# Optimization experiments

Hardware: AMD Instinct MI355X
Metric: run time of the kernel (lower is better)

The kernel has to match this reference:

```python
import jax, jax.numpy as jnp
import numpy as np

D_MODEL = 1024
NUM_LAYERS = 4
VOCAB = 32000
NUM_HEADS = 8
HEAD_DIM = D_MODEL // NUM_HEADS
FFN_DIM = 2048
BATCH = 4
SEQ = 1024
LN_EPS = 1e-5
ROPE_THETA = 10000.0


def setup_inputs() -> dict:
    key = jax.random.key(0)
    ks = iter(jax.random.split(key, 32))
    std = 0.02
    L, D, H, Dh, F, V = NUM_LAYERS, D_MODEL, NUM_HEADS, HEAD_DIM, FFN_DIM, VOCAB
    inp = {
        "tokens": jax.random.randint(next(ks), (BATCH, SEQ), 0, V, dtype=jnp.int32),
        "emb": jax.random.normal(next(ks), (V, D), jnp.float32),
        # per-layer stacked params; Linear weights stored pre-transposed (in, out)
        "Wqkv": jax.random.normal(next(ks), (L, D, 3 * D), jnp.float32) * std,
        "bqkv": jnp.zeros((L, 3 * D), jnp.float32),
        "Wo": jax.random.normal(next(ks), (L, D, D), jnp.float32) * std,
        "bo": jnp.zeros((L, D), jnp.float32),
        "ln1_g": jnp.ones((L, D), jnp.float32),
        "ln1_b": jnp.zeros((L, D), jnp.float32),
        "ln2_g": jnp.ones((L, D), jnp.float32),
        "ln2_b": jnp.zeros((L, D), jnp.float32),
        "W1": jax.random.normal(next(ks), (L, D, F), jnp.float32) * std,
        "b1": jnp.zeros((L, F), jnp.float32),
        "W2": jax.random.normal(next(ks), (L, F, D), jnp.float32) * std,
        "b2": jnp.zeros((L, D), jnp.float32),
        "lnf_g": jnp.ones((D,), jnp.float32),
        "lnf_b": jnp.zeros((D,), jnp.float32),
        "Wout": jax.random.normal(next(ks), (D, V), jnp.float32) * std,
        "bout": jnp.zeros((V,), jnp.float32),
    }
    return inp


def _layernorm(x, g, b):
    mu = jnp.mean(x, -1, keepdims=True)
    var = jnp.mean(jnp.square(x - mu), -1, keepdims=True)
    return (x - mu) * jax.lax.rsqrt(var + LN_EPS) * g + b


def _rope_cos_sin(seq, dh, dtype):
    inv_freq = 1.0 / (ROPE_THETA ** (jnp.arange(0, dh, 2, dtype=jnp.float32) / dh))
    t = jnp.arange(seq, dtype=jnp.float32)
    freqs = jnp.outer(t, inv_freq)                      # [S, Dh/2]
    emb = jnp.concatenate([freqs, freqs], axis=-1)      # [S, Dh]
    return jnp.cos(emb).astype(dtype), jnp.sin(emb).astype(dtype)


def _rotate_half(x):
    x1, x2 = jnp.split(x, 2, axis=-1)
    return jnp.concatenate([-x2, x1], axis=-1)


def _apply_rope(x, cos, sin):
    # x: [B,S,H,Dh]; cos/sin: [S,Dh] -> broadcast over batch and heads
    return x * cos[None, :, None, :] + _rotate_half(x) * sin[None, :, None, :]


def reference(tokens, emb, Wqkv, bqkv, Wo, bo, ln1_g, ln1_b, ln2_g, ln2_b,
              W1, b1, W2, b2, lnf_g, lnf_b, Wout, bout):
    B, S = tokens.shape
    H, Dh = NUM_HEADS, HEAD_DIM
    x = emb[tokens]                                      # [B,S,D]
    cos, sin = _rope_cos_sin(S, Dh, x.dtype)
    causal = jnp.tril(jnp.ones((S, S), dtype=bool))      # True = keep
    scale = 1.0 / jnp.sqrt(jnp.asarray(Dh, x.dtype))

    def layer(xc, p):
        (wqkv, bq, wo, bo_, g1, b1_, g2, b2_, w1, bb1, w2, bb2) = p
        y = _layernorm(xc, g1, b1_)
        qkv = (y @ wqkv + bq).reshape(B, S, 3, H, Dh)
        q, k, v = qkv[:, :, 0], qkv[:, :, 1], qkv[:, :, 2]
        q = _apply_rope(q, cos, sin)
        k = _apply_rope(k, cos, sin)
        scores = jnp.einsum("bshd,bthd->bhst", q, k) * scale
        scores = jnp.where(causal[None, None], scores, -jnp.inf)
        attn = jax.nn.softmax(scores, axis=-1)
        ctx = jnp.einsum("bhst,bthd->bshd", attn, v).reshape(B, S, H * Dh)
        xc = xc + ctx @ wo + bo_
        z = _layernorm(xc, g2, b2_)
        ff = jax.nn.gelu(z @ w1 + bb1, approximate=False) @ w2 + bb2
        return xc + ff, None

    params = (Wqkv, bqkv, Wo, bo, ln1_g, ln1_b, ln2_g, ln2_b, W1, b1, W2, b2)
    x, _ = jax.lax.scan(layer, x, params)
    x = _layernorm(x, lnf_g, lnf_b)
    return x @ Wout + bout                                # [B,S,V]
```

## Files before the change

kernel.cpp:

```cpp
#include <hip/hip_runtime.h>
#include <hip/hip_bf16.h>
#include <math.h>


#define D_MODEL 1024
#define SEQ     1024
#define BATCH   4
#define NHEAD   8
#define HDIM    128
#define FFN     2048
#define NLAYER  4
#define VOCAB   32000
#define MROWS   (BATCH*SEQ)

typedef unsigned short ushort_t;
typedef __attribute__((ext_vector_type(8))) short s16x8;
typedef __attribute__((ext_vector_type(4))) float f32x4;

__device__ __forceinline__ ushort_t f2bf(float f) {
    union { float f; unsigned int u; } c; c.f = f;
    unsigned int u = c.u;
    unsigned int r = (u + 0x7FFFu + ((u >> 16) & 1u)) >> 16;
    return (ushort_t)r;
}
__device__ __forceinline__ float bf2f(ushort_t u) {
    union { unsigned int u; float f; } c; c.u = ((unsigned int)u) << 16; return c.f;
}

__device__ __forceinline__ void gload16(const void* g, void* l) {
    __builtin_amdgcn_global_load_lds(
        (const __attribute__((address_space(1))) unsigned int*)g,
        (__attribute__((address_space(3))) unsigned int*)l, 16, 0, 0);
}

__device__ __forceinline__ float gelu_exact(float x) {
    return 0.5f * x * (1.0f + erff(x * 0.70710678118654752f));
}

__global__ __launch_bounds__(256) void embed_kernel(
    const int* __restrict__ tokens, const float* __restrict__ emb,
    float* __restrict__ X)
{
    int row = blockIdx.x;
    int t = tokens[row];
    const float4* src = (const float4*)(emb + (size_t)t * D_MODEL);
    float4* dst = (float4*)(X + (size_t)row * D_MODEL);
    dst[threadIdx.x] = src[threadIdx.x];
}

__global__ __launch_bounds__(256) void ln_kernel(
    const float* __restrict__ X, const float* __restrict__ g,
    const float* __restrict__ b, ushort_t* __restrict__ Y)
{
    __shared__ float red[8];
    int row = blockIdx.x;
    const float4* x4 = (const float4*)(X + (size_t)row * D_MODEL);
    float4 v = x4[threadIdx.x];
    float s  = v.x + v.y + v.z + v.w;
    float ss = v.x*v.x + v.y*v.y + v.z*v.z + v.w*v.w;
    #pragma unroll
    for (int o = 32; o > 0; o >>= 1) { s += __shfl_down(s, o); ss += __shfl_down(ss, o); }
    int wid = threadIdx.x >> 6;
    if ((threadIdx.x & 63) == 0) { red[wid] = s; red[wid + 4] = ss; }
    __syncthreads();
    float tot  = red[0] + red[1] + red[2] + red[3];
    float tot2 = red[4] + red[5] + red[6] + red[7];
    float mu  = tot * (1.0f / D_MODEL);
    float var = tot2 * (1.0f / D_MODEL) - mu * mu;
    float r = rsqrtf(var + 1e-5f);
    const float4* g4 = (const float4*)g;
    const float4* b4 = (const float4*)b;
    float4 gv = g4[threadIdx.x], bv = b4[threadIdx.x];
    ushort4 o;
    o.x = f2bf((v.x - mu) * r * gv.x + bv.x);
    o.y = f2bf((v.y - mu) * r * gv.y + bv.y);
    o.z = f2bf((v.z - mu) * r * gv.z + bv.z);
    o.w = f2bf((v.w - mu) * r * gv.w + bv.w);
    ((ushort4*)(Y + (size_t)row * D_MODEL))[threadIdx.x] = o;
}

__global__ __launch_bounds__(256) void wconv(
    const float* __restrict__ W, ushort_t* __restrict__ Wt, int K, int N)
{
    __shared__ float t[32][33];
    const float* Wl = W + (size_t)blockIdx.z * K * N;
    ushort_t* Wtl = Wt + (size_t)blockIdx.z * K * N;
    int k0 = blockIdx.y * 32, n0 = blockIdx.x * 32;
    int tid = threadIdx.x;
    int r = tid >> 3, c4 = (tid & 7) * 4;
    float4 v = *(const float4*)(Wl + (size_t)(k0 + r) * N + n0 + c4);
    t[r][c4+0] = v.x; t[r][c4+1] = v.y; t[r][c4+2] = v.z; t[r][c4+3] = v.w;
    __syncthreads();
    ushort4 o;
    o.x = f2bf(t[c4+0][r]); o.y = f2bf(t[c4+1][r]);
    o.z = f2bf(t[c4+2][r]); o.w = f2bf(t[c4+3][r]);
    *(ushort4*)(Wtl + (size_t)(n0 + r) * K + k0 + c4) = o;
}

template<int ACT, int BETA, int OBF>
__global__ __launch_bounds__(256) void gemm_mid(
    const ushort_t* __restrict__ A, const ushort_t* __restrict__ Bt,
    const float* __restrict__ bias, float* __restrict__ Cf,
    ushort_t* __restrict__ Cb, int M, int N, int K)
{
    __shared__ __align__(16) ushort_t As[2][128 * 64];
    __shared__ __align__(16) ushort_t Bs[2][128 * 64];
    int tid = threadIdx.x, lane = tid & 63, w = tid >> 6;
    int wm = w >> 1, wn = w & 1;
    int m0 = blockIdx.x * 128, n0 = blockIdx.y * 128;
    int lr = lane & 15, kg = lane >> 4;
    const int NKT = K / 64;

    f32x4 acc[4][4] = {};

    int srow = w * 8 + (lane >> 3);
    int scol = (((lane & 7) ^ ((lane >> 3) & 7))) * 8;

    int rsw = lr & 7;
    int ch0 = (kg    ) ^ rsw;
    int ch1 = (kg + 4) ^ rsw;

#define STAGE_A(db, ht, ktile) do { \
    const ushort_t* s_ = A + (size_t)(m0 + (ht) * 64 + srow) * K + (size_t)(ktile) * 64 + scol; \
    gload16(s_,                  &As[db][((ht) * 64 + w * 8) * 64]); \
    gload16(s_ + (size_t)32 * K, &As[db][((ht) * 64 + 32 + w * 8) * 64]); \
} while (0)
#define STAGE_B(db, ht, ktile) do { \
    const ushort_t* s_ = Bt + (size_t)(n0 + (ht) * 64 + srow) * K + (size_t)(ktile) * 64 + scol; \
    gload16(s_,                  &Bs[db][((ht) * 64 + w * 8) * 64]); \
    gload16(s_ + (size_t)32 * K, &Bs[db][((ht) * 64 + 32 + w * 8) * 64]); \
} while (0)
#define SBAR() do { __builtin_amdgcn_sched_barrier(0); \
    __builtin_amdgcn_s_barrier(); __builtin_amdgcn_sched_barrier(0); } while (0)

    STAGE_A(0, 0, 0); STAGE_A(0, 1, 0); STAGE_B(0, 0, 0); STAGE_B(0, 1, 0);
    STAGE_A(1, 0, 1);
    asm volatile("s_waitcnt vmcnt(2)" ::: "memory");
    SBAR();

    for (int kt = 0; kt < NKT; ++kt) {
        int d = kt & 1, dn = d ^ 1;
        const ushort_t* pa0 = &As[d][(wm * 64 + lr) * 64 + ch0 * 8];
        const ushort_t* pa1 = &As[d][(wm * 64 + lr) * 64 + ch1 * 8];
        const ushort_t* pb0 = &Bs[d][(wn * 64 + lr) * 64 + ch0 * 8];
        const ushort_t* pb1 = &Bs[d][(wn * 64 + lr) * 64 + ch1 * 8];
        s16x8 a[4][2], b[4][2];

        #pragma unroll
        for (int mi = 0; mi < 4; ++mi) {
            a[mi][0] = *(const s16x8*)(pa0 + mi * 1024);
            a[mi][1] = *(const s16x8*)(pa1 + mi * 1024);
        }
        #pragma unroll
        for (int ni = 0; ni < 4; ++ni) {
            b[ni][0] = *(const s16x8*)(pb0 + ni * 1024);
            b[ni][1] = *(const s16x8*)(pb1 + ni * 1024);
        }
        if (kt + 1 < NKT) STAGE_A(dn, 1, kt + 1);
        __builtin_amdgcn_sched_barrier(0);

        __builtin_amdgcn_s_setprio(1);
        #pragma unroll
        for (int mi = 0; mi < 2; ++mi)
            #pragma unroll
            for (int ni = 0; ni < 2; ++ni)
                #pragma unroll
                for (int kk = 0; kk < 2; ++kk)
                    acc[mi][ni] = __builtin_amdgcn_mfma_f32_16x16x32_bf16(
                        a[mi][kk], b[ni][kk], acc[mi][ni], 0, 0, 0);
        __builtin_amdgcn_s_setprio(0);
        __builtin_amdgcn_sched_barrier(0);
        if (kt + 1 < NKT) STAGE_B(dn, 0, kt + 1);
        __builtin_amdgcn_sched_barrier(0);

        __builtin_amdgcn_s_setprio(1);
        #pragma unroll
        for (int mi = 0; mi < 2; ++mi)
            #pragma unroll
            for (int ni = 2; ni < 4; ++ni)
                #pragma unroll
                for (int kk = 0; kk < 2; ++kk)
                    acc[mi][ni] = __builtin_amdgcn_mfma_f32_16x16x32_bf16(
                        a[mi][kk], b[ni][kk], acc[mi][ni], 0, 0, 0);
        __builtin_amdgcn_s_setprio(0);
        __builtin_amdgcn_sched_barrier(0);
        if (kt + 1 < NKT) STAGE_B(dn, 1, kt + 1);
        __builtin_amdgcn_sched_barrier(0);

        __builtin_amdgcn_s_setprio(1);
        #pragma unroll
        for (int mi = 2; mi < 4; ++mi)
            #pragma unroll
            for (int ni = 0; ni < 2; ++ni)
                #pragma unroll
                for (int kk = 0; kk < 2; ++kk)
                    acc[mi][ni] = __builtin_amdgcn_mfma_f32_16x16x32_bf16(
                        a[mi][kk], b[ni][kk], acc[mi][ni], 0, 0, 0);
        __builtin_amdgcn_s_setprio(0);

        asm volatile("s_waitcnt lgkmcnt(0)" ::: "memory");
        SBAR();
        if (kt + 2 < NKT) STAGE_A(d, 0, kt + 2);
        __builtin_amdgcn_sched_barrier(0);

        __builtin_amdgcn_s_setprio(1);
        #pragma unroll
        for (int mi = 2; mi < 4; ++mi)
            #pragma unroll
            for (int ni = 2; ni < 4; ++ni)
                #pragma unroll
                for (int kk = 0; kk < 2; ++kk)
                    acc[mi][ni] = __builtin_amdgcn_mfma_f32_16x16x32_bf16(
                        a[mi][kk], b[ni][kk], acc[mi][ni], 0, 0, 0);
        __builtin_amdgcn_s_setprio(0);

        if (kt + 2 < NKT) {
            asm volatile("s_waitcnt vmcnt(2)" ::: "memory");
        } else {
            asm volatile("s_waitcnt vmcnt(0)" ::: "memory");
        }
        SBAR();
    }
#undef STAGE_A
#undef STAGE_B
#undef SBAR

    #pragma unroll
    for (int mi = 0; mi < 4; ++mi) {
        int rbase = m0 + wm * 64 + mi * 16 + kg * 4;
        #pragma unroll
        for (int ni = 0; ni < 4; ++ni) {
            int col = n0 + wn * 64 + ni * 16 + lr;
            float bz = bias[col];
            f32x4 v = acc[mi][ni];
            #pragma unroll
            for (int j = 0; j < 4; ++j) {
                float x = v[j] + bz;
                if (ACT == 1) x = gelu_exact(x);
                size_t off = (size_t)(rbase + j) * N + col;
                if (OBF) {
                    Cb[off] = f2bf(x);
                } else {
                    if (BETA) x += Cf[off];
                    Cf[off] = x;
                }
            }
        }
    }
}

__global__ __launch_bounds__(512) void gemm_big(
    const ushort_t* __restrict__ A, const ushort_t* __restrict__ Bt,
    const float* __restrict__ bias, float* __restrict__ C,
    int M, int N, int K)
{
    __shared__ __align__(16) ushort_t As[2][256 * 64];
    __shared__ __align__(16) ushort_t Bs[2][256 * 64];
    int tid = threadIdx.x, lane = tid & 63, w = tid >> 6;
    int wm = w >> 2, wn = w & 3;
    int m0 = blockIdx.x * 256, n0 = blockIdx.y * 256;
    int lr = lane & 15, kg = lane >> 4;
    const int NKT = K / 64;

    f32x4 acc[8][4] = {};

    int srow = w * 8 + (lane >> 3);
    int scol = (((lane & 7) ^ ((lane >> 3) & 7))) * 8;

    int rsw = lr & 7;
    int ch0 = (kg    ) ^ rsw;
    int ch1 = (kg + 4) ^ rsw;

#define STAGE_A(db, ht, ktile) do { \
    const ushort_t* s_ = A + (size_t)(m0 + (ht) * 128 + srow) * K + (size_t)(ktile) * 64 + scol; \
    gload16(s_,                  &As[db][((ht) * 128 + w * 8) * 64]); \
    gload16(s_ + (size_t)64 * K, &As[db][((ht) * 128 + 64 + w * 8) * 64]); \
} while (0)
#define STAGE_B(db, ht, ktile) do { \
    const ushort_t* s_ = Bt + (size_t)(n0 + (ht) * 128 + srow) * K + (size_t)(ktile) * 64 + scol; \
    gload16(s_,                  &Bs[db][((ht) * 128 + w * 8) * 64]); \
    gload16(s_ + (size_t)64 * K, &Bs[db][((ht) * 128 + 64 + w * 8) * 64]); \
} while (0)
#define SBAR() do { __builtin_amdgcn_sched_barrier(0); \
    __builtin_amdgcn_s_barrier(); __builtin_amdgcn_sched_barrier(0); } while (0)

    STAGE_A(0, 0, 0); STAGE_A(0, 1, 0); STAGE_B(0, 0, 0); STAGE_B(0, 1, 0);
    STAGE_A(1, 0, 1);
    asm volatile("s_waitcnt vmcnt(2)" ::: "memory");
    SBAR();

    for (int kt = 0; kt < NKT; ++kt) {
        int d = kt & 1, dn = d ^ 1;
        const ushort_t* pa0 = &As[d][(wm * 128 + lr) * 64 + ch0 * 8];
        const ushort_t* pa1 = &As[d][(wm * 128 + lr) * 64 + ch1 * 8];
        const ushort_t* pb0 = &Bs[d][(wn * 64  + lr) * 64 + ch0 * 8];
        const ushort_t* pb1 = &Bs[d][(wn * 64  + lr) * 64 + ch1 * 8];
        s16x8 a03[4][2], a47[4][2], b01[2][2], b23[2][2];

        #pragma unroll
        for (int mi = 0; mi < 4; ++mi) {
            a03[mi][0] = *(const s16x8*)(pa0 + mi * 1024);
            a03[mi][1] = *(const s16x8*)(pa1 + mi * 1024);
        }
        #pragma unroll
        for (int ni = 0; ni < 2; ++ni) {
            b01[ni][0] = *(const s16x8*)(pb0 + ni * 1024);
            b01[ni][1] = *(const s16x8*)(pb1 + ni * 1024);
        }
        #pragma unroll
        for (int ni = 0; ni < 2; ++ni) {
            b23[ni][0] = *(const s16x8*)(pb0 + (2 + ni) * 1024);
            b23[ni][1] = *(const s16x8*)(pb1 + (2 + ni) * 1024);
        }
        #pragma unroll
        for (int mi = 0; mi < 4; ++mi) {
            a47[mi][0] = *(const s16x8*)(pa0 + (4 + mi) * 1024);
            a47[mi][1] = *(const s16x8*)(pa1 + (4 + mi) * 1024);
        }
        if (kt + 1 < NKT) STAGE_A(dn, 1, kt + 1);
        __builtin_amdgcn_sched_barrier(0);

        __builtin_amdgcn_s_setprio(1);
        #pragma unroll
        for (int mi = 0; mi < 4; ++mi)
            #pragma unroll
            for (int ni = 0; ni < 2; ++ni)
                #pragma unroll
                for (int kk = 0; kk < 2; ++kk)
                    acc[mi][ni] = __builtin_amdgcn_mfma_f32_16x16x32_bf16(
                        a03[mi][kk], b01[ni][kk], acc[mi][ni], 0, 0, 0);
        __builtin_amdgcn_s_setprio(0);
        __builtin_amdgcn_sched_barrier(0);
        if (kt + 1 < NKT) STAGE_B(dn, 0, kt + 1);
        __builtin_amdgcn_sched_barrier(0);

        __builtin_amdgcn_s_setprio(1);
        #pragma unroll
        for (int mi = 0; mi < 4; ++mi)
            #pragma unroll
            for (int ni = 0; ni < 2; ++ni)
                #pragma unroll
                for (int kk = 0; kk < 2; ++kk)
                    acc[mi][2 + ni] = __builtin_amdgcn_mfma_f32_16x16x32_bf16(
                        a03[mi][kk], b23[ni][kk], acc[mi][2 + ni], 0, 0, 0);
        __builtin_amdgcn_s_setprio(0);
        __builtin_amdgcn_sched_barrier(0);
        if (kt + 1 < NKT) STAGE_B(dn, 1, kt + 1);
        __builtin_amdgcn_sched_barrier(0);

        __builtin_amdgcn_s_setprio(1);
        #pragma unroll
        for (int mi = 0; mi < 4; ++mi)
            #pragma unroll
            for (int ni = 0; ni < 2; ++ni)
                #pragma unroll
                for (int kk = 0; kk < 2; ++kk)
                    acc[4 + mi][ni] = __builtin_amdgcn_mfma_f32_16x16x32_bf16(
                        a47[mi][kk], b01[ni][kk], acc[4 + mi][ni], 0, 0, 0);
        __builtin_amdgcn_s_setprio(0);

        asm volatile("s_waitcnt lgkmcnt(0)" ::: "memory");
        SBAR();
        if (kt + 2 < NKT) STAGE_A(d, 0, kt + 2);
        __builtin_amdgcn_sched_barrier(0);

        __builtin_amdgcn_s_setprio(1);
        #pragma unroll
        for (int mi = 0; mi < 4; ++mi)
            #pragma unroll
            for (int ni = 0; ni < 2; ++ni)
                #pragma unroll
                for (int kk = 0; kk < 2; ++kk)
                    acc[4 + mi][2 + ni] = __builtin_amdgcn_mfma_f32_16x16x32_bf16(
                        a47[mi][kk], b23[ni][kk], acc[4 + mi][2 + ni], 0, 0, 0);
        __builtin_amdgcn_s_setprio(0);

        if (kt + 2 < NKT) {
            asm volatile("s_waitcnt vmcnt(2)" ::: "memory");
        } else {
            asm volatile("s_waitcnt vmcnt(0)" ::: "memory");
        }
        SBAR();
    }
#undef STAGE_A
#undef STAGE_B
#undef SBAR

    #pragma unroll
    for (int mi = 0; mi < 8; ++mi) {
        int rbase = m0 + wm * 128 + mi * 16 + kg * 4;
        #pragma unroll
        for (int ni = 0; ni < 4; ++ni) {
            int col = n0 + wn * 64 + ni * 16 + lr;
            float bz = bias[col];
            f32x4 v = acc[mi][ni];
            #pragma unroll
            for (int j = 0; j < 4; ++j)
                C[(size_t)(rbase + j) * N + col] = v[j] + bz;
        }
    }
}

__global__ __launch_bounds__(64) void rope_table_kernel(float2* __restrict__ RT)
{
    int s = blockIdx.x, p = threadIdx.x;
    float inv = expf(-0.14391156831212788f * (float)p);
    float ang = (float)s * inv;
    float sn, c;
    sincosf(ang, &sn, &c);
    RT[s * 64 + p] = make_float2(c, sn);
}

__global__ __launch_bounds__(256) void ropeq_kernel(
    const ushort_t* __restrict__ QKVb, const float2* __restrict__ RT,
    ushort_t* __restrict__ Qb, ushort_t* __restrict__ Kb)
{
    int m = blockIdx.x;
    int b = m >> 10, s = m & (SEQ - 1);
    const ushort_t* rowbase = QKVb + (size_t)m * (3 * D_MODEL);
    const float2* t2 = RT + s * 64;
    int tid = threadIdx.x;
    int qk = tid >> 7;
    int rem = tid & 127;
    int hh = rem >> 4;
    int p4 = (rem & 15) * 4;
    const ushort_t* base = rowbase + qk * D_MODEL + hh * HDIM + p4;
    ushort4 lo = *(const ushort4*)base;
    ushort4 hi = *(const ushort4*)(base + 64);
    ushort_t lov[4] = {lo.x, lo.y, lo.z, lo.w};
    ushort_t hiv[4] = {hi.x, hi.y, hi.z, hi.w};
    ushort_t lor[4], hir[4];
    #pragma unroll
    for (int j = 0; j < 4; ++j) {
        float2 cs = t2[p4 + j];
        float x1 = bf2f(lov[j]), x2 = bf2f(hiv[j]);
        lor[j] = f2bf(x1 * cs.x - x2 * cs.y);
        hir[j] = f2bf(x2 * cs.x + x1 * cs.y);
    }
    ushort_t* dst = (qk ? Kb : Qb) + ((size_t)(b * NHEAD + hh) * SEQ + s) * HDIM + p4;
    *(ushort4*)dst        = make_ushort4(lor[0], lor[1], lor[2], lor[3]);
    *(ushort4*)(dst + 64) = make_ushort4(hir[0], hir[1], hir[2], hir[3]);
}

__global__ __launch_bounds__(256) void vtrans_kernel(
    const ushort_t* __restrict__ QKVb, ushort_t* __restrict__ Vt)
{
    __shared__ ushort_t tl[64][34];
    int s0 = blockIdx.x * 64;
    int d0 = blockIdx.y * 32;
    int b  = blockIdx.z;
    int tid = threadIdx.x;
    #pragma unroll
    for (int r = 0; r < 4; ++r) {
        int li = tid + r * 256;
        int row = li >> 4;
        int cp  = (li & 15) * 2;
        ushort2 v = *(const ushort2*)(QKVb + (size_t)(b * SEQ + s0 + row) * 3072
                                      + 2 * D_MODEL + d0 + cp);
        tl[row][cp]     = v.x;
        tl[row][cp + 1] = v.y;
    }
    __syncthreads();
    #pragma unroll
    for (int r = 0; r < 4; ++r) {
        int li = tid + r * 256;
        int drow = li >> 5;
        int sc   = (li & 31) * 2;
        ushort2 o;
        o.x = tl[sc][drow];
        o.y = tl[sc + 1][drow];
        *(ushort2*)(Vt + (size_t)(b * D_MODEL + d0 + drow) * SEQ + s0 + sc) = o;
    }
}

#define PSTR 72

__global__ __launch_bounds__(256) void attn_mfma(
    const ushort_t* __restrict__ Qb, const ushort_t* __restrict__ Kb,
    const ushort_t* __restrict__ Vt, ushort_t* __restrict__ Yb)
{
    __shared__ __align__(16) ushort_t Ks[64 * 136];
    __shared__ __align__(16) ushort_t Vts[128 * 72];
    __shared__ __align__(16) ushort_t Pl[4][16 * PSTR];
    int bid = blockIdx.x;
    int qt = bid & 15, h = (bid >> 4) & 7, b = bid >> 7;
    int q0 = qt * 64;
    int tid = threadIdx.x, lane = tid & 63, w = tid >> 6;
    int lr = lane & 15, g = lane >> 4;
    const float scale = 0.08838834764831845f;

    const ushort_t* Qbase = Qb + (size_t)((b * NHEAD + h) * SEQ) * HDIM;
    const ushort_t* Kbase = Kb + (size_t)((b * NHEAD + h) * SEQ) * HDIM;
    const ushort_t* Vbase = Vt + (size_t)(b * D_MODEL + h * HDIM) * SEQ;

    s16x8 aq[4];
    #pragma unroll
    for (int kc = 0; kc < 4; ++kc)
        aq[kc] = *(const s16x8*)(Qbase + (size_t)(q0 + w * 16 + lr) * HDIM + kc * 32 + g * 8);

    f32x4 acc_o[8] = {};
    float mx[4] = {-INFINITY, -INFINITY, -INFINITY, -INFINITY};
    float ls[4] = {};

    int ntiles = q0 / 64 + 1;
    for (int t = 0; t < ntiles; ++t) {
        int j0 = t * 64;
        __syncthreads();
        #pragma unroll
        for (int r = 0; r < 4; ++r) {
            int idx = tid + r * 256;
            int row = idx >> 4, c16 = idx & 15;
            *(s16x8*)&Ks[row * 136 + c16 * 8] =
                *(const s16x8*)(Kbase + (size_t)(j0 + row) * HDIM + c16 * 8);
        }
        #pragma unroll
        for (int r = 0; r < 4; ++r) {
            int idx = tid + r * 256;
            int row = idx >> 3, c8 = idx & 7;
            *(s16x8*)&Vts[row * 72 + c8 * 8] =
                *(const s16x8*)(Vbase + (size_t)row * SEQ + j0 + c8 * 8);
        }
        __syncthreads();

        f32x4 sa[4] = {};
        __builtin_amdgcn_s_setprio(1);
        #pragma unroll
        for (int nb = 0; nb < 4; ++nb)
            #pragma unroll
            for (int kc = 0; kc < 4; ++kc) {
                s16x8 bk = *(const s16x8*)&Ks[(nb * 16 + lr) * 136 + kc * 32 + g * 8];
                sa[nb] = __builtin_amdgcn_mfma_f32_16x16x32_bf16(aq[kc], bk, sa[nb], 0, 0, 0);
            }
        __builtin_amdgcn_s_setprio(0);

        bool diag = (j0 == q0);
        float pv[4][4];
        #pragma unroll
        for (int nb = 0; nb < 4; ++nb)
            #pragma unroll
            for (int j = 0; j < 4; ++j) {
                float v = sa[nb][j] * scale;
                if (diag) {
                    int kv = j0 + nb * 16 + lr;
                    int qq = q0 + w * 16 + g * 4 + j;
                    if (kv > qq) v = -INFINITY;
                }
                pv[nb][j] = v;
            }
        #pragma unroll
        for (int j = 0; j < 4; ++j) {
            float tm = fmaxf(fmaxf(pv[0][j], pv[1][j]), fmaxf(pv[2][j], pv[3][j]));
            #pragma unroll
            for (int o = 1; o < 16; o <<= 1) tm = fmaxf(tm, __shfl_xor(tm, o));
            float nm = fmaxf(mx[j], tm);
            float corr = expf(mx[j] - nm);
            float ts = 0.0f;
            #pragma unroll
            for (int nb = 0; nb < 4; ++nb) {
                float e = expf(pv[nb][j] - nm);
                pv[nb][j] = e;
                ts += e;
            }
            #pragma unroll
            for (int o = 1; o < 16; o <<= 1) ts += __shfl_xor(ts, o);
            ls[j] = ls[j] * corr + ts;
            mx[j] = nm;
            #pragma unroll
            for (int dn = 0; dn < 8; ++dn) acc_o[dn][j] *= corr;
        }
        #pragma unroll
        for (int nb = 0; nb < 4; ++nb)
            #pragma unroll
            for (int j = 0; j < 4; ++j)
                Pl[w][(g * 4 + j) * PSTR + nb * 16 + lr] = f2bf(pv[nb][j]);
        #pragma unroll
        for (int kk = 0; kk < 2; ++kk) {
            s16x8 pa = *(const s16x8*)&Pl[w][lr * PSTR + kk * 32 + g * 8];
            __builtin_amdgcn_s_setprio(1);
            #pragma unroll
            for (int dn = 0; dn < 8; ++dn) {
                s16x8 bv = *(const s16x8*)&Vts[(dn * 16 + lr) * 72 + kk * 32 + g * 8];
                acc_o[dn] = __builtin_amdgcn_mfma_f32_16x16x32_bf16(pa, bv, acc_o[dn], 0, 0, 0);
            }
            __builtin_amdgcn_s_setprio(0);
        }
    }

    float il[4];
    #pragma unroll
    for (int j = 0; j < 4; ++j) il[j] = 1.0f / ls[j];
    #pragma unroll
    for (int dn = 0; dn < 8; ++dn)
        #pragma unroll
        for (int j = 0; j < 4; ++j) {
            int q = q0 + w * 16 + g * 4 + j;
            Yb[(size_t)(b * SEQ + q) * D_MODEL + h * HDIM + dn * 16 + lr] =
                f2bf(acc_o[dn][j] * il[j]);
        }
}

extern "C" void kernel_launch(void* const* d_in, const int* in_sizes, int n_in,
                              void* d_out, int out_size, void* d_ws, size_t ws_size,
                              hipStream_t stream)
{
    const int*   tokens = (const int*)  d_in[0];
    const float* emb    = (const float*)d_in[1];
    const float* Wqkv   = (const float*)d_in[2];
    const float* bqkv   = (const float*)d_in[3];
    const float* Wo     = (const float*)d_in[4];
    const float* bo     = (const float*)d_in[5];
    const float* ln1_g  = (const float*)d_in[6];
    const float* ln1_b  = (const float*)d_in[7];
    const float* ln2_g  = (const float*)d_in[8];
    const float* ln2_b  = (const float*)d_in[9];
    const float* W1     = (const float*)d_in[10];
    const float* b1     = (const float*)d_in[11];
    const float* W2     = (const float*)d_in[12];
    const float* b2     = (const float*)d_in[13];
    const float* lnf_g  = (const float*)d_in[14];
    const float* lnf_b  = (const float*)d_in[15];
    const float* Wout   = (const float*)d_in[16];
    const float* bout   = (const float*)d_in[17];
    float* out = (float*)d_out;

    char* ws = (char*)d_ws;
    float*    X      = (float*)ws;
    ushort_t* Abuf   = (ushort_t*)(ws + 16777216);
    ushort_t* QKVb   = (ushort_t*)(ws + 25165824);
    ushort_t* Gbuf   = (ushort_t*)(ws + 25165824);
    ushort_t* Qbb    = (ushort_t*)(ws + 50331648);
    ushort_t* Kbb    = (ushort_t*)(ws + 58720256);
    ushort_t* Vtb    = (ushort_t*)(ws + 67108864);
    ushort_t* WqkvT  = (ushort_t*)(ws + 75497472);
    ushort_t* WoT    = (ushort_t*)(ws + 100663296);
    ushort_t* W1T    = (ushort_t*)(ws + 109051904);
    ushort_t* W2T    = (ushort_t*)(ws + 125829120);
    ushort_t* WoutT  = (ushort_t*)(ws + 142606336);
    float2*   RT     = (float2*)  (ws + 208142336);

    const int M = MROWS, Dm = D_MODEL, F = FFN, V = VOCAB;

    rope_table_kernel<<<SEQ, 64, 0, stream>>>(RT);

    wconv<<<dim3(3*Dm/32, Dm/32, NLAYER), 256, 0, stream>>>(Wqkv, WqkvT, Dm, 3*Dm);
    wconv<<<dim3(Dm/32,   Dm/32, NLAYER), 256, 0, stream>>>(Wo,   WoT,   Dm, Dm);
    wconv<<<dim3(F/32,    Dm/32, NLAYER), 256, 0, stream>>>(W1,   W1T,   Dm, F);
    wconv<<<dim3(Dm/32,   F/32,  NLAYER), 256, 0, stream>>>(W2,   W2T,   F,  Dm);
    wconv<<<dim3(V/32,    Dm/32, 1),      256, 0, stream>>>(Wout, WoutT, Dm, V);

    embed_kernel<<<MROWS, 256, 0, stream>>>(tokens, emb, X);

    for (int L = 0; L < NLAYER; ++L) {
        ln_kernel<<<MROWS, 256, 0, stream>>>(X, ln1_g + (size_t)L*Dm, ln1_b + (size_t)L*Dm, Abuf);
        gemm_mid<0,0,1><<<dim3(M/128, 3*Dm/128), 256, 0, stream>>>(
            Abuf, WqkvT + (size_t)L*3*Dm*Dm, bqkv + (size_t)L*3*Dm, nullptr, QKVb, M, 3*Dm, Dm);
        ropeq_kernel<<<MROWS, 256, 0, stream>>>(QKVb, RT, Qbb, Kbb);
        vtrans_kernel<<<dim3(SEQ/64, Dm/32, BATCH), 256, 0, stream>>>(QKVb, Vtb);
        attn_mfma<<<BATCH*NHEAD*(SEQ/64), 256, 0, stream>>>(Qbb, Kbb, Vtb, Abuf);
        gemm_mid<0,1,0><<<dim3(M/128, Dm/128), 256, 0, stream>>>(
            Abuf, WoT + (size_t)L*Dm*Dm, bo + (size_t)L*Dm, X, nullptr, M, Dm, Dm);
        ln_kernel<<<MROWS, 256, 0, stream>>>(X, ln2_g + (size_t)L*Dm, ln2_b + (size_t)L*Dm, Abuf);
        gemm_mid<1,0,1><<<dim3(M/128, F/128), 256, 0, stream>>>(
            Abuf, W1T + (size_t)L*Dm*F, b1 + (size_t)L*F, nullptr, Gbuf, M, F, Dm);
        gemm_mid<0,1,0><<<dim3(M/128, Dm/128), 256, 0, stream>>>(
            Gbuf, W2T + (size_t)L*F*Dm, b2 + (size_t)L*Dm, X, nullptr, M, Dm, F);
    }

    ln_kernel<<<MROWS, 256, 0, stream>>>(X, lnf_g, lnf_b, Abuf);
    gemm_big<<<dim3(M/256, V/256), 512, 0, stream>>>(
        Abuf, WoutT, bout, out, M, V, Dm);
}
```

Baseline: 1.383 ms.

## Prefetch next K/V tile into registers and lazily rescale softmax

The attention loop now loads the next K and V tile from global memory into registers while the current tile is computed, then writes them to shared memory at the start of the next iteration. This hides global load latency behind MFMA and softmax work. The online softmax now rescales the running max and accumulators only when the new tile max exceeds the old one by more than 8, skipping most per-tile exp and multiply work. In exchange it uses more registers, and unnormalized probabilities can grow up to about e^8 before bf16 conversion.

```diff
diff --git a/kernel.cpp b/kernel.cpp
--- a/kernel.cpp
+++ b/kernel.cpp
@@ -498,27 +498,39 @@
     for (int kc = 0; kc < 4; ++kc)
         aq[kc] = *(const s16x8*)(Qbase + (size_t)(q0 + w * 16 + lr) * HDIM + kc * 32 + g * 8);
 
+    int krow = tid >> 4, kc16 = tid & 15;
+    int vrow = tid >> 3, vc8  = tid & 7;
+
     f32x4 acc_o[8] = {};
     float mx[4] = {-INFINITY, -INFINITY, -INFINITY, -INFINITY};
     float ls[4] = {};
+
+    s16x8 kreg[4], vreg[4];
+    #pragma unroll
+    for (int r = 0; r < 4; ++r)
+        kreg[r] = *(const s16x8*)(Kbase + (size_t)(krow + r * 16) * HDIM + kc16 * 8);
+    #pragma unroll
+    for (int r = 0; r < 4; ++r)
+        vreg[r] = *(const s16x8*)(Vbase + (size_t)(vrow + r * 32) * SEQ + vc8 * 8);
 
     int ntiles = q0 / 64 + 1;
     for (int t = 0; t < ntiles; ++t) {
         int j0 = t * 64;
         __syncthreads();
         #pragma unroll
-        for (int r = 0; r < 4; ++r) {
-            int idx = tid + r * 256;
-            int row = idx >> 4, c16 = idx & 15;
-            *(s16x8*)&Ks[row * 136 + c16 * 8] =
-                *(const s16x8*)(Kbase + (size_t)(j0 + row) * HDIM + c16 * 8);
-        }
-        #pragma unroll
-        for (int r = 0; r < 4; ++r) {
-            int idx = tid + r * 256;
-            int row = idx >> 3, c8 = idx & 7;
-            *(s16x8*)&Vts[row * 72 + c8 * 8] =
-                *(const s16x8*)(Vbase + (size_t)row * SEQ + j0 + c8 * 8);
+        for (int r = 0; r < 4; ++r)
+            *(s16x8*)&Ks[(krow + r * 16) * 136 + kc16 * 8] = kreg[r];
+        #pragma unroll
+        for (int r = 0; r < 4; ++r)
+            *(s16x8*)&Vts[(vrow + r * 32) * 72 + vc8 * 8] = vreg[r];
+        if (t + 1 < ntiles) {
+            int jn = j0 + 64;
+            #pragma unroll
+            for (int r = 0; r < 4; ++r)
+                kreg[r] = *(const s16x8*)(Kbase + (size_t)(jn + krow + r * 16) * HDIM + kc16 * 8);
+            #pragma unroll
+            for (int r = 0; r < 4; ++r)
+                vreg[r] = *(const s16x8*)(Vbase + (size_t)(vrow + r * 32) * SEQ + jn + vc8 * 8);
         }
         __syncthreads();
 
@@ -552,21 +564,23 @@
             float tm = fmaxf(fmaxf(pv[0][j], pv[1][j]), fmaxf(pv[2][j], pv[3][j]));
             #pragma unroll
             for (int o = 1; o < 16; o <<= 1) tm = fmaxf(tm, __shfl_xor(tm, o));
-            float nm = fmaxf(mx[j], tm);
-            float corr = expf(mx[j] - nm);
+            if (tm > mx[j] + 8.0f) {
+                float corr = expf(mx[j] - tm);
+                mx[j] = tm;
+                ls[j] *= corr;
+                #pragma unroll
+                for (int dn = 0; dn < 8; ++dn) acc_o[dn][j] *= corr;
+            }
             float ts = 0.0f;
             #pragma unroll
             for (int nb = 0; nb < 4; ++nb) {
-                float e = expf(pv[nb][j] - nm);
+                float e = expf(pv[nb][j] - mx[j]);
                 pv[nb][j] = e;
                 ts += e;
             }
             #pragma unroll
             for (int o = 1; o < 16; o <<= 1) ts += __shfl_xor(ts, o);
-            ls[j] = ls[j] * corr + ts;
-            mx[j] = nm;
-            #pragma unroll
-            for (int dn = 0; dn < 8; ++dn) acc_o[dn][j] *= corr;
+            ls[j] += ts;
         }
         #pragma unroll
         for (int nb = 0; nb < 4; ++nb)
```

New measurement: 1.379 ms. Within noise of the previous version (-0.3%).
